# Performance work log

Hardware: AMD Instinct MI355X
Metric: run time of the kernel (lower is better)

## Reference

```python
import jax, jax.numpy as jnp
import numpy as np

B, S, D = 524288, 10, 6  # batch of independent tiny attention problems; original module is one [10,6] sample


def setup_inputs() -> dict:
    key = jax.random.key(0)
    ks = jax.random.split(key, 7)
    bound = 1.0 / np.sqrt(D)  # torch nn.Linear default init range
    x = jax.random.normal(ks[0], (B, S, D), dtype=jnp.float32)
    Wk = jax.random.uniform(ks[1], (D, D), jnp.float32, -bound, bound)
    bk = jax.random.uniform(ks[2], (D,), jnp.float32, -bound, bound)
    Wq = jax.random.uniform(ks[3], (D, D), jnp.float32, -bound, bound)
    bq = jax.random.uniform(ks[4], (D,), jnp.float32, -bound, bound)
    Wv = jax.random.uniform(ks[5], (D, D), jnp.float32, -bound, bound)
    bv = jax.random.uniform(ks[6], (D,), jnp.float32, -bound, bound)
    return {"x": x, "Wk": Wk, "bk": bk, "Wq": Wq, "bq": bq, "Wv": Wv, "bv": bv}


def reference(x, Wk, bk, Wq, bq, Wv, bv):
    # Linear layers (torch stores W as [out,in]; y = x W^T + b)
    k = jnp.einsum('bsd,ed->bse', x, Wk) + bk  # [B,S,D]
    q = jnp.einsum('bsd,ed->bse', x, Wq) + bq
    v = jnp.einsum('bsd,ed->bse', x, Wv) + bv
    # per-query attention over the 10 keys (no scaling in original)
    scores = jax.nn.softmax(jnp.einsum('bqd,bkd->bqk', q, k), axis=-1)  # [B,S,S]
    out = jnp.einsum('bqk,bkd->bqd', scores, v)  # [B,S,D]
    # original sums attended vector over feature dim -> one scalar per query
    return jnp.sum(out, axis=-1)  # [B,S]
```

## Files before the change

### kernel.cpp

```cpp
#include <hip/hip_runtime.h>


#define NB 524288
#define S 10
#define D 6
#define TPB 256
#define EPB 128
#define ROW 61

__global__ void precompute_kernel(const float* __restrict__ Wk, const float* __restrict__ bk,
                                  const float* __restrict__ Wq, const float* __restrict__ bq,
                                  const float* __restrict__ Wv, const float* __restrict__ bv,
                                  float* __restrict__ ws) {
    int t = threadIdx.x;
    if (t < 36) {
        int d = t / 6, dp = t % 6;
        float g = 0.f;
        for (int e = 0; e < D; ++e) g += Wq[e * D + d] * Wk[e * D + dp];
        ws[t] = g;
    } else if (t < 42) {
        int dp = t - 36;
        float s = 0.f;
        for (int e = 0; e < D; ++e) s += bq[e] * Wk[e * D + dp];
        ws[t] = s;
    } else if (t < 48) {
        int d = t - 42;
        float s = 0.f;
        for (int e = 0; e < D; ++e) s += Wv[e * D + d];
        ws[t] = s;
    } else if (t == 48) {
        float s = 0.f;
        for (int e = 0; e < D; ++e) s += bv[e];
        ws[t] = s;
    }
}

__global__ __launch_bounds__(TPB, 4) void attn_kernel(const float* __restrict__ x,
                                                      const float* __restrict__ ws,
                                                      float* __restrict__ out) {
    __shared__ float xs[EPB * ROW];
    const int t = threadIdx.x;
    const int blk = blockIdx.x;

    float G[36], w[6], wvs[6];
    #pragma unroll
    for (int i = 0; i < 36; ++i) G[i] = ws[i];
    #pragma unroll
    for (int i = 0; i < 6; ++i) w[i] = ws[36 + i];
    #pragma unroll
    for (int i = 0; i < 6; ++i) wvs[i] = ws[42 + i];
    const float bvs = ws[48];

    const float4* xg = (const float4*)x + (size_t)blk * (EPB * 15);
    #pragma unroll
    for (int i = 0; i < 8; ++i) {
        int f = t + TPB * i;
        if (f < EPB * 15) {
            float4 v = xg[f];
            int e = f / 15, sub = f - e * 15;
            float* dst = &xs[e * ROW + sub * 4];
            dst[0] = v.x; dst[1] = v.y; dst[2] = v.z; dst[3] = v.w;
        }
    }
    __syncthreads();

    const int e = t >> 1;
    const int h = t & 1;
    const float* xe = &xs[e * ROW];

    float tq[5][6];
    #pragma unroll
    for (int j = 0; j < 5; ++j) {
        int q = h * 5 + j;
        float xq[6];
        #pragma unroll
        for (int d = 0; d < 6; ++d) xq[d] = xe[q * 6 + d];
        #pragma unroll
        for (int dp = 0; dp < 6; ++dp) {
            float s = 0.f;
            #pragma unroll
            for (int d = 0; d < 6; ++d) s += xq[d] * G[d * 6 + dp];
            tq[j][dp] = s;
        }
    }

    float num[5] = {0.f, 0.f, 0.f, 0.f, 0.f};
    float den[5] = {0.f, 0.f, 0.f, 0.f, 0.f};
    #pragma unroll
    for (int k = 0; k < S; ++k) {
        float xk[6];
        #pragma unroll
        for (int d = 0; d < 6; ++d) xk[d] = xe[k * 6 + d];
        float a = 0.f, vk = bvs;
        #pragma unroll
        for (int d = 0; d < 6; ++d) { a += w[d] * xk[d]; vk += wvs[d] * xk[d]; }
        #pragma unroll
        for (int j = 0; j < 5; ++j) {
            float s = a;
            #pragma unroll
            for (int d = 0; d < 6; ++d) s += tq[j][d] * xk[d];
            float ex = __expf(s);
            den[j] += ex;
            num[j] += ex * vk;
        }
    }

    float* op = out + (size_t)blk * (EPB * S) + t * 5;
    #pragma unroll
    for (int j = 0; j < 5; ++j) op[j] = num[j] * __builtin_amdgcn_rcpf(den[j]);
}

extern "C" void kernel_launch(void* const* d_in, const int* in_sizes, int n_in,
                              void* d_out, int out_size, void* d_ws, size_t ws_size,
                              hipStream_t stream) {
    const float* x  = (const float*)d_in[0];
    const float* Wk = (const float*)d_in[1];
    const float* bk = (const float*)d_in[2];
    const float* Wq = (const float*)d_in[3];
    const float* bq = (const float*)d_in[4];
    const float* Wv = (const float*)d_in[5];
    const float* bv = (const float*)d_in[6];
    float* out = (float*)d_out;
    float* ws  = (float*)d_ws;

    precompute_kernel<<<1, 64, 0, stream>>>(Wk, bk, Wq, bq, Wv, bv, ws);
    attn_kernel<<<NB / EPB, TPB, 0, stream>>>(x, ws, out);
}
```

Measured before the change: 43.86 us.

## Stage x into LDS with direct global-to-LDS loads and fold log2e into weights

Replaces the register-staged float4 copy into a padded LDS buffer with global_load_lds DMA-style loads into an unpadded buffer, overlapping the copy with the loads of the weight matrix. Each thread then reads its whole 60-float row from LDS with vectorized float4 loads instead of scalar reads. The exp is switched to the native exp2, with log2(e) folded into the precomputed G and bias terms so no multiply is needed per exponent. Removing the padding may bring back LDS bank conflicts on the row-per-thread float4 reads, and holding the full row in registers raises register pressure.

```diff
diff --git a/kernel.cpp b/kernel.cpp
--- a/kernel.cpp
+++ b/kernel.cpp
@@ -6,23 +6,25 @@
 #define D 6
 #define TPB 256
 #define EPB 128
-#define ROW 61
+#define XFL (S * D)
+#define LDS_FLOATS (EPB * XFL)
 
 __global__ void precompute_kernel(const float* __restrict__ Wk, const float* __restrict__ bk,
                                   const float* __restrict__ Wq, const float* __restrict__ bq,
                                   const float* __restrict__ Wv, const float* __restrict__ bv,
                                   float* __restrict__ ws) {
+    const float LOG2E = 1.44269504088896340736f;
     int t = threadIdx.x;
     if (t < 36) {
         int d = t / 6, dp = t % 6;
         float g = 0.f;
         for (int e = 0; e < D; ++e) g += Wq[e * D + d] * Wk[e * D + dp];
-        ws[t] = g;
+        ws[t] = g * LOG2E;
     } else if (t < 42) {
         int dp = t - 36;
         float s = 0.f;
         for (int e = 0; e < D; ++e) s += bq[e] * Wk[e * D + dp];
-        ws[t] = s;
+        ws[t] = s * LOG2E;
     } else if (t < 48) {
         int d = t - 42;
         float s = 0.f;
@@ -38,9 +40,23 @@
 __global__ __launch_bounds__(TPB, 4) void attn_kernel(const float* __restrict__ x,
                                                       const float* __restrict__ ws,
                                                       float* __restrict__ out) {
-    __shared__ float xs[EPB * ROW];
+    __shared__ float xs[LDS_FLOATS];
     const int t = threadIdx.x;
     const int blk = blockIdx.x;
+    const int wave = t >> 6;
+    const int lane = t & 63;
+
+    const float* gbase = x + (size_t)blk * LDS_FLOATS;
+    #pragma unroll
+    for (int i = 0; i < 8; ++i) {
+        int c = wave + 4 * i;
+        if (c < 30) {
+            __builtin_amdgcn_global_load_lds(
+                (const __attribute__((address_space(1))) void*)(gbase + c * 256 + lane * 4),
+                (__attribute__((address_space(3))) void*)(&xs[c * 256 + lane * 4]),
+                16, 0, 0);
+        }
+    }
 
     float G[36], w[6], wvs[6];
     #pragma unroll
@@ -51,35 +67,30 @@
     for (int i = 0; i < 6; ++i) wvs[i] = ws[42 + i];
     const float bvs = ws[48];
 
-    const float4* xg = (const float4*)x + (size_t)blk * (EPB * 15);
-    #pragma unroll
-    for (int i = 0; i < 8; ++i) {
-        int f = t + TPB * i;
-        if (f < EPB * 15) {
-            float4 v = xg[f];
-            int e = f / 15, sub = f - e * 15;
-            float* dst = &xs[e * ROW + sub * 4];
-            dst[0] = v.x; dst[1] = v.y; dst[2] = v.z; dst[3] = v.w;
-        }
-    }
     __syncthreads();
 
     const int e = t >> 1;
     const int h = t & 1;
-    const float* xe = &xs[e * ROW];
+
+    float xv[XFL];
+    const float4* xr = (const float4*)&xs[e * XFL];
+    #pragma unroll
+    for (int i = 0; i < 15; ++i) {
+        float4 v = xr[i];
+        xv[4 * i + 0] = v.x;
+        xv[4 * i + 1] = v.y;
+        xv[4 * i + 2] = v.z;
+        xv[4 * i + 3] = v.w;
+    }
 
     float tq[5][6];
     #pragma unroll
     for (int j = 0; j < 5; ++j) {
-        int q = h * 5 + j;
-        float xq[6];
-        #pragma unroll
-        for (int d = 0; d < 6; ++d) xq[d] = xe[q * 6 + d];
         #pragma unroll
         for (int dp = 0; dp < 6; ++dp) {
             float s = 0.f;
             #pragma unroll
-            for (int d = 0; d < 6; ++d) s += xq[d] * G[d * 6 + dp];
+            for (int d = 0; d < 6; ++d) s += xv[(h * 5 + j) * 6 + d] * G[d * 6 + dp];
             tq[j][dp] = s;
         }
     }
@@ -88,18 +99,18 @@
     float den[5] = {0.f, 0.f, 0.f, 0.f, 0.f};
     #pragma unroll
     for (int k = 0; k < S; ++k) {
-        float xk[6];
-        #pragma unroll
-        for (int d = 0; d < 6; ++d) xk[d] = xe[k * 6 + d];
         float a = 0.f, vk = bvs;
         #pragma unroll
-        for (int d = 0; d < 6; ++d) { a += w[d] * xk[d]; vk += wvs[d] * xk[d]; }
+        for (int d = 0; d < 6; ++d) {
+            a += w[d] * xv[k * 6 + d];
+            vk += wvs[d] * xv[k * 6 + d];
+        }
         #pragma unroll
         for (int j = 0; j < 5; ++j) {
             float s = a;
             #pragma unroll
-            for (int d = 0; d < 6; ++d) s += tq[j][d] * xk[d];
-            float ex = __expf(s);
+            for (int d = 0; d < 6; ++d) s += tq[j][d] * xv[k * 6 + d];
+            float ex = __builtin_amdgcn_exp2f(s);
             den[j] += ex;
             num[j] += ex * vk;
         }
```

Result: slower. 101.6 us (+131.7%).
